# Kernel tuning notes

Measured on AMD Instinct MI355X. Metric: run time of the kernel, lower is better.

The kernel has to match this reference:

```python
import jax, jax.numpy as jnp
import numpy as np

EPS = 1e-5

def channel_norm(x):
    # per-(batch,channel) norm over spatial dims; torch.var default is unbiased (ddof=1)
    mn = x.mean(axis=(-1, -2), keepdims=True)
    std = jnp.sqrt(x.var(axis=(-1, -2), keepdims=True, ddof=1) + EPS)
    return (x - mn) / std

def conv1x1(x, W, b):
    # x: [B,C,H,W], W: [O,C], b: [O]
    return jnp.einsum('oc,bchw->bohw', W, x) + b[None, :, None, None]

def setup_inputs() -> dict:
    key = jax.random.key(0)
    ks = jax.random.split(key, 10)
    B, C, H, W = 4, 512, 64, 64
    s = 1.0 / np.sqrt(C)  # kaiming-uniform-ish scale for 1x1 conv
    inp = {
        'f_c': jax.random.normal(ks[0], (B, C, H, W), jnp.float32),
        'f_s': jax.random.normal(ks[1], (B, C, H, W), jnp.float32),
        'W_c1': jax.random.uniform(ks[2], (C, C), jnp.float32, -s, s),
        'b_c1': jax.random.uniform(ks[3], (C,), jnp.float32, -s, s),
        'W_s1': jax.random.uniform(ks[4], (C, C), jnp.float32, -s, s),
        'b_s1': jax.random.uniform(ks[5], (C,), jnp.float32, -s, s),
        'W_s2': jax.random.uniform(ks[6], (C, C), jnp.float32, -s, s),
        'b_s2': jax.random.uniform(ks[7], (C,), jnp.float32, -s, s),
        'W_csc': jax.random.uniform(ks[8], (C, C), jnp.float32, -s, s),
        'b_csc': jax.random.uniform(ks[9], (C,), jnp.float32, -s, s),
    }
    return inp

def reference(f_c, f_s, W_c1, b_c1, W_s1, b_s1, W_s2, b_s2, W_csc, b_csc):
    B, C, H, W = f_c.shape
    f_c_hat = channel_norm(f_c)
    f_s_hat = channel_norm(f_s)
    f = conv1x1(f_c_hat, W_c1, b_c1).reshape(B, C, H * W)  # queries [B,C,N]
    g = conv1x1(f_s_hat, W_s1, b_s1).reshape(B, C, H * W)  # keys    [B,C,N]
    scores = jnp.einsum('bci,bcj->bij', f, g)              # [B,N,N]
    attention = jax.nn.softmax(scores, axis=-1)
    h = conv1x1(f_s_hat, W_s2, b_s2).reshape(B, C, H * W)  # values  [B,C,N]
    out = jnp.einsum('bcj,bij->bci', h, attention).reshape(B, C, H, W)
    return conv1x1(out, W_csc, b_csc) + f_c
```

## Files before the change

### kernel.cpp

```cpp
#include <hip/hip_runtime.h>

typedef unsigned short u16;
typedef __attribute__((ext_vector_type(8))) _Float16 f16x8;
typedef __attribute__((ext_vector_type(16))) float f32x16;

#define N_SP 4096
#define C_CH 512
#define B_SZ 4

struct PtrTab { u16* p[4]; };

__device__ __forceinline__ u16 f2h(float f) {
    union { _Float16 h; u16 u; } x; x.h = (_Float16)f; return x.u;
}
__device__ __forceinline__ float h2f(u16 u) {
    union { u16 u; _Float16 h; } x; x.u = u; return (float)x.h;
}
__device__ __forceinline__ void async_cp16(const void* g, void* l) {
    __builtin_amdgcn_global_load_lds((const __attribute__((address_space(1))) unsigned*)g,
                                     (__attribute__((address_space(3))) unsigned*)l, 16, 0, 0);
}
__device__ __forceinline__ float wave_reduce_sum(float v) {
    #pragma unroll
    for (int off = 32; off; off >>= 1) v += __shfl_xor(v, off, 64);
    return v;
}
__device__ __forceinline__ float wave_reduce_max(float v) {
    #pragma unroll
    for (int off = 32; off; off >>= 1) v = fmaxf(v, __shfl_xor(v, off, 64));
    return v;
}

__global__ __launch_bounds__(256) void transpose_cast_stats(
        const float* __restrict__ fc, const float* __restrict__ fs,
        u16* __restrict__ xc, u16* __restrict__ xs,
        float* __restrict__ part_s, float* __restrict__ part_ss) {
    __shared__ float tile[64][65];
    const int t = threadIdx.x;
    const int n0 = blockIdx.x * 64, c0 = blockIdx.y * 64;
    const int z = blockIdx.z;
    const int b = z & 3, which = z >> 2;
    const float* src = which ? fs : fc;
    u16* dst = which ? xs : xc;
    const int r = t >> 4, q4 = (t & 15) * 4;
    #pragma unroll
    for (int it = 0; it < 4; ++it) {
        const int row = it * 16 + r;
        float4 v = *(const float4*)(src + ((size_t)b * C_CH + c0 + row) * N_SP + n0 + q4);
        tile[row][q4 + 0] = v.x; tile[row][q4 + 1] = v.y;
        tile[row][q4 + 2] = v.z; tile[row][q4 + 3] = v.w;
    }
    __syncthreads();
    {
        const int cr = t >> 2, q = t & 3;
        float s = 0.f, ss = 0.f;
        #pragma unroll
        for (int i = 0; i < 16; ++i) {
            float a = tile[cr][q * 16 + i];
            s += a; ss += a * a;
        }
        s += __shfl_xor(s, 1, 64);  s += __shfl_xor(s, 2, 64);
        ss += __shfl_xor(ss, 1, 64); ss += __shfl_xor(ss, 2, 64);
        if (q == 0) {
            atomicAdd(&part_s[z * 512 + c0 + cr], s);
            atomicAdd(&part_ss[z * 512 + c0 + cr], ss);
        }
    }
    #pragma unroll
    for (int it = 0; it < 4; ++it) {
        const int nrow = it * 16 + r;
        ushort4 h4;
        h4.x = f2h(tile[q4 + 0][nrow]);
        h4.y = f2h(tile[q4 + 1][nrow]);
        h4.z = f2h(tile[q4 + 2][nrow]);
        h4.w = f2h(tile[q4 + 3][nrow]);
        *(ushort4*)(dst + ((size_t)b * N_SP + n0 + nrow) * C_CH + c0 + q4) = h4;
    }
}

__global__ __launch_bounds__(256) void prep1(
        const float* __restrict__ W_c1, const float* __restrict__ W_s1,
        const float* __restrict__ W_s2, const float* __restrict__ W_csc,
        const float* __restrict__ b_c1, const float* __restrict__ b_s2,
        const float* __restrict__ b_csc,
        u16* __restrict__ Wbase,
        const float* __restrict__ part_s, const float* __restrict__ part_ss,
        float* __restrict__ mu_a, float* __restrict__ rs_a,
        float* __restrict__ w_u, float* __restrict__ bfold0) {
    __shared__ float tile[64][65];
    const int t = threadIdx.x, z = blockIdx.z;
    if (z < 4) {
        const int n0 = blockIdx.x * 64, c0 = blockIdx.y * 64;
        const float* W = (z == 0) ? W_c1 : (z == 1) ? W_s1 : (z == 2) ? W_s2 : W_csc;
        u16* D = Wbase + ((z == 0) ? 2 : (z == 1) ? 0 : (z == 2) ? 3 : 1) * 262144;
        const int r = t >> 4, q4 = (t & 15) * 4;
        #pragma unroll
        for (int it = 0; it < 4; ++it) {
            const int row = it * 16 + r;
            float4 v = *(const float4*)(W + (size_t)(c0 + row) * 512 + n0 + q4);
            if (z == 3) {
                ushort4 h4 = { f2h(v.x), f2h(v.y), f2h(v.z), f2h(v.w) };
                *(ushort4*)(D + (size_t)(c0 + row) * 512 + n0 + q4) = h4;
            } else {
                tile[row][q4 + 0] = v.x; tile[row][q4 + 1] = v.y;
                tile[row][q4 + 2] = v.z; tile[row][q4 + 3] = v.w;
            }
        }
        __syncthreads();
        if (z == 3) return;
        #pragma unroll
        for (int it = 0; it < 4; ++it) {
            const int nrow = it * 16 + r;
            ushort4 h4;
            h4.x = f2h(tile[q4 + 0][nrow]);
            h4.y = f2h(tile[q4 + 1][nrow]);
            h4.z = f2h(tile[q4 + 2][nrow]);
            h4.w = f2h(tile[q4 + 3][nrow]);
            *(ushort4*)(D + (size_t)(n0 + nrow) * 512 + c0 + q4) = h4;
        }
        return;
    }
    const int flat = blockIdx.y * 8 + blockIdx.x;
    if (flat < 8) {
        #pragma unroll
        for (int h = 0; h < 2; ++h) {
            const int c = flat * 512 + h * 256 + t;
            const float S = part_s[c], SS = part_ss[c];
            const float mean = S * (1.f / N_SP);
            const float var = (SS - S * mean) * (1.f / (N_SP - 1));
            mu_a[c] = mean;
            rs_a[c] = rsqrtf(var + 1e-5f);
        }
    } else if (flat < 10) {
        const int d = (flat - 8) * 256 + t;
        float acc = 0.f;
        for (int o = 0; o < 512; ++o) acc += b_c1[o] * W_s1[(size_t)o * 512 + d];
        w_u[d] = acc;
    } else if (flat < 42) {
        const int w4 = t >> 6, l = t & 63;
        #pragma unroll
        for (int q = 0; q < 4; ++q) {
            const int o = (flat - 10) * 16 + w4 * 4 + q;
            const float4 w0 = *(const float4*)(W_csc + (size_t)o * 512 + l * 8);
            const float4 w1 = *(const float4*)(W_csc + (size_t)o * 512 + l * 8 + 4);
            const float4 b0 = *(const float4*)(b_s2 + l * 8);
            const float4 b1 = *(const float4*)(b_s2 + l * 8 + 4);
            float acc = w0.x * b0.x + w0.y * b0.y + w0.z * b0.z + w0.w * b0.w
                      + w1.x * b1.x + w1.y * b1.y + w1.z * b1.z + w1.w * b1.w;
            acc = wave_reduce_sum(acc);
            if (l == 0) bfold0[o] = acc + b_csc[o];
        }
    }
}

__global__ __launch_bounds__(256) void prep2(
        const u16* __restrict__ WqT16, const u16* __restrict__ Wf16,
        const u16* __restrict__ xs,
        const float* __restrict__ mu_a, const float* __restrict__ rs_a,
        const float* __restrict__ bfold0, const float* __restrict__ w_u,
        u16* __restrict__ Wq_z, u16* __restrict__ Wf_z,
        float* __restrict__ bq, float* __restrict__ bh, float* __restrict__ u_) {
    const int id = blockIdx.x, t = threadIdx.x;
    if (id < 1024) {
        const int y = id >> 9;
        const size_t e = ((size_t)(id & 511) * 256 + t) * 8;
        const int z = (int)(e >> 18), rem = (int)(e & 262143);
        const int d = rem >> 9, a0 = rem & 511;
        u16 v[8];
        if (y == 0) {
            *(uint4*)v = *(const uint4*)(WqT16 + rem);
            const float rd = rs_a[(4 + z) * 512 + d];
            const float* rc = rs_a + z * 512 + a0;
            #pragma unroll
            for (int i = 0; i < 8; ++i) v[i] = f2h(h2f(v[i]) * rc[i] * rd);
            *(uint4*)(Wq_z + e) = *(const uint4*)v;
        } else {
            *(uint4*)v = *(const uint4*)(Wf16 + rem);
            const float* rk = rs_a + (4 + z) * 512 + a0;
            #pragma unroll
            for (int i = 0; i < 8; ++i) v[i] = f2h(h2f(v[i]) * rk[i]);
            *(uint4*)(Wf_z + e) = *(const uint4*)v;
        }
    } else if (id < 2048) {
        const int w = t >> 6, l = t & 63;
        const int oid = (id - 1024) * 4 + w;
        const int kind = oid >> 11;
        const int z = (oid >> 9) & 3, d = oid & 511;
        const u16* row = (kind == 0 ? WqT16 : Wf16) + (size_t)d * 512;
        const int sb = (kind == 0 ? z : 4 + z) * 512;
        float acc = 0.f;
        #pragma unroll
        for (int i = 0; i < 8; ++i) {
            const int a = l * 8 + i;
            acc += h2f(row[a]) * mu_a[sb + a] * rs_a[sb + a];
        }
        acc = wave_reduce_sum(acc);
        if (l == 0) {
            if (kind == 0) bq[z * 512 + d] = -acc * rs_a[(4 + z) * 512 + d];
            else           bh[z * 512 + d] = bfold0[d] - acc;
        }
    } else {
        const int id2 = id - 2048;
        const int b = id2 >> 6, xblk = id2 & 63;
        const int w = t >> 6, l = t & 63;
        float4 u0 = *(const float4*)(w_u + l * 8);
        float4 u1 = *(const float4*)(w_u + l * 8 + 4);
        const float4 r0 = *(const float4*)(rs_a + (4 + b) * 512 + l * 8);
        const float4 r1 = *(const float4*)(rs_a + (4 + b) * 512 + l * 8 + 4);
        u0.x *= r0.x; u0.y *= r0.y; u0.z *= r0.z; u0.w *= r0.w;
        u1.x *= r1.x; u1.y *= r1.y; u1.z *= r1.z; u1.w *= r1.w;
        #pragma unroll
        for (int jj = 0; jj < 16; ++jj) {
            const int j = xblk * 64 + w * 16 + jj;
            const u16* row = xs + ((size_t)b * N_SP + j) * C_CH + l * 8;
            f16x8 x = *(const f16x8*)row;
            float acc = (float)x[0] * u0.x + (float)x[1] * u0.y + (float)x[2] * u0.z + (float)x[3] * u0.w
                      + (float)x[4] * u1.x + (float)x[5] * u1.y + (float)x[6] * u1.z + (float)x[7] * u1.w;
            acc = wave_reduce_sum(acc);
            if (l == 0) u_[(size_t)b * N_SP + j] = acc;
        }
    }
}

enum { OUT_F32 = 0, OUT_F16 = 1 };

template<int OUTMODE, bool TABB, bool TABD, int MI, int MJ>
__global__ __launch_bounds__(256) void gemm_bt(
    const u16* __restrict__ A, const u16* __restrict__ B, PtrTab tab,
    float* __restrict__ Df, u16* __restrict__ Dh,
    const float* __restrict__ bias_m, const float* __restrict__ bias_n,
    const float* __restrict__ res,
    int M, int N, int K, int lda, int ldb, int ldd,
    size_t sA, size_t sB, size_t sD, size_t sR, int sBm, int sBn)
{
    constexpr int TM = MI * 64, TN = MJ * 64, BK = 64;
    constexpr int AITS = (TM * BK) / (256 * 8);
    constexpr int BITS = (TN * BK) / (256 * 8);
    __shared__ u16 smem[(TM + TN) * BK];
    u16* As = smem;
    u16* Bs = smem + TM * BK;

    const int t = threadIdx.x;
    const int l = t & 63, w = t >> 6;
    const int m0 = blockIdx.y * TM, n0 = blockIdx.x * TN;
    const size_t zb = blockIdx.z;
    const u16* pA = A + zb * sA + (size_t)m0 * lda;
    const u16* pB = (TABB ? tab.p[zb] : B + zb * sB) + (size_t)n0 * ldb;

    const int wr = (w & 1) * (MI * 32), wc = (w >> 1) * (MJ * 32);

    f32x16 acc[MI][MJ] = {};

    for (int k0 = 0; k0 < K; k0 += BK) {
        #pragma unroll
        for (int it = 0; it < AITS; ++it) {
            const int L = it * 256 + t;
            const int row = L >> 3, c = L & 7;
            const int sc = (c ^ (row & 7)) * 8;
            async_cp16(pA + (size_t)row * lda + k0 + sc, As + L * 8);
        }
        #pragma unroll
        for (int it = 0; it < BITS; ++it) {
            const int L = it * 256 + t;
            const int row = L >> 3, c = L & 7;
            const int sc = (c ^ (row & 7)) * 8;
            async_cp16(pB + (size_t)row * ldb + k0 + sc, Bs + L * 8);
        }
        __syncthreads();
        #pragma unroll
        for (int kk = 0; kk < 4; ++kk) {
            f16x8 af[MI], bf[MJ];
            #pragma unroll
            for (int i = 0; i < MI; ++i) {
                const int row = wr + i * 32 + (l & 31);
                const int ch = ((kk * 2 + (l >> 5)) ^ (row & 7)) * 8;
                af[i] = *(const f16x8*)(As + row * BK + ch);
            }
            #pragma unroll
            for (int j = 0; j < MJ; ++j) {
                const int row = wc + j * 32 + (l & 31);
                const int ch = ((kk * 2 + (l >> 5)) ^ (row & 7)) * 8;
                bf[j] = *(const f16x8*)(Bs + row * BK + ch);
            }
            #pragma unroll
            for (int i = 0; i < MI; ++i)
                #pragma unroll
                for (int j = 0; j < MJ; ++j)
                    acc[i][j] = __builtin_amdgcn_mfma_f32_32x32x16_f16(af[i], bf[j], acc[i][j], 0, 0, 0);
        }
        __syncthreads();
    }

    const int cl = l & 31, rh = (l >> 5) * 4;
    u16* pDh = (OUTMODE == OUT_F16) ? (TABD ? tab.p[zb] : Dh + zb * sD) : nullptr;
    float* pDf = (OUTMODE == OUT_F32) ? (Df + zb * sD) : nullptr;
    #pragma unroll
    for (int i = 0; i < MI; ++i) {
        #pragma unroll
        for (int j = 0; j < MJ; ++j) {
            const int nn = n0 + wc + j * 32 + cl;
            const float bn = bias_n ? bias_n[(size_t)sBn * zb + nn] : 0.f;
            #pragma unroll
            for (int reg = 0; reg < 16; ++reg) {
                const int ml = (reg & 3) + 8 * (reg >> 2) + rh;
                const int mm = m0 + wr + i * 32 + ml;
                float v = acc[i][j][reg] + bn;
                if (bias_m) v += bias_m[(size_t)sBm * zb + mm];
                const size_t off = (size_t)mm * ldd + nn;
                if (OUTMODE == OUT_F32) {
                    if (res) v += res[zb * sR + off];
                    pDf[off] = v;
                } else {
                    pDh[off] = f2h(v);
                }
            }
        }
    }
}

__global__ __launch_bounds__(256) void softmax_kernel(PtrTab tab) {
    u16* row = tab.p[blockIdx.y] + (size_t)blockIdx.x * N_SP;
    const int t = threadIdx.x;
    u16 raw[16];
    *(uint4*)(raw + 0) = *(const uint4*)(row + t * 16);
    *(uint4*)(raw + 8) = *(const uint4*)(row + t * 16 + 8);
    float v[16];
    float mx = -1e30f;
    #pragma unroll
    for (int i = 0; i < 16; ++i) { v[i] = h2f(raw[i]); mx = fmaxf(mx, v[i]); }
    mx = wave_reduce_max(mx);
    __shared__ float red[4];
    const int wave = t >> 6;
    if ((t & 63) == 0) red[wave] = mx;
    __syncthreads();
    mx = fmaxf(fmaxf(red[0], red[1]), fmaxf(red[2], red[3]));
    float sum = 0.f;
    #pragma unroll
    for (int i = 0; i < 16; ++i) { v[i] = __expf(v[i] - mx); sum += v[i]; }
    sum = wave_reduce_sum(sum);
    __syncthreads();
    if ((t & 63) == 0) red[wave] = sum;
    __syncthreads();
    const float inv = 1.f / (red[0] + red[1] + red[2] + red[3]);
    #pragma unroll
    for (int i = 0; i < 16; ++i) raw[i] = f2h(v[i] * inv);
    *(uint4*)(row + t * 16)     = *(const uint4*)(raw + 0);
    *(uint4*)(row + t * 16 + 8) = *(const uint4*)(raw + 8);
}

extern "C" void kernel_launch(void* const* d_in, const int* in_sizes, int n_in,
                              void* d_out, int out_size, void* d_ws, size_t ws_size,
                              hipStream_t stream) {
    const float* f_c   = (const float*)d_in[0];
    const float* f_s   = (const float*)d_in[1];
    const float* W_c1  = (const float*)d_in[2];
    const float* b_c1  = (const float*)d_in[3];
    const float* W_s1  = (const float*)d_in[4];
    const float* b_s1  = (const float*)d_in[5]; (void)b_s1;
    const float* W_s2  = (const float*)d_in[6];
    const float* b_s2  = (const float*)d_in[7];
    const float* W_csc = (const float*)d_in[8];
    const float* b_csc = (const float*)d_in[9];

    const size_t PB = (size_t)N_SP * C_CH;
    const size_t M1 = 1024 * 1024;

    u16* ws   = (u16*)d_ws;
    u16* Xs   = ws;
    u16* q_   = ws + 8 * M1;
    u16* hc   = ws + 16 * M1;
    u16* Xc   = ws + 24 * M1;
    u16* S3   = ws + 24 * M1;
    u16* S0   = ws + 40 * M1;
    u16* S1   = ws + 56 * M1;
    u16* S2   = ws + 72 * M1;
    u16* Wbase= ws + 88 * M1;
    u16* WqT16= Wbase + 4 * 262144;
    u16* Wf16 = Wbase + 5 * 262144;
    u16* Wq_z = Wbase + 6 * 262144;
    u16* Wf_z = Wq_z + 1048576;
    float* f32b = (float*)(ws + 92 * M1);
    float* part_s  = f32b;
    float* part_ss = f32b + 4096;
    float* mu_a    = f32b + 8192;
    float* rs_a    = f32b + 12288;
    float* w_u     = f32b + 16384;
    float* bfold0  = f32b + 16896;
    float* bq      = f32b + 17408;
    float* bh      = f32b + 19456;
    float* u_      = f32b + 21504;

    PtrTab Stab; Stab.p[0] = S0; Stab.p[1] = S1; Stab.p[2] = S2; Stab.p[3] = S3;
    PtrTab tab0 = Stab;

    hipMemsetAsync(part_s, 0, 2 * 4096 * sizeof(float), stream);

    transpose_cast_stats<<<dim3(64, 8, 8), 256, 0, stream>>>(f_c, f_s, Xc, Xs, part_s, part_ss);

    prep1<<<dim3(8, 8, 5), 256, 0, stream>>>(W_c1, W_s1, W_s2, W_csc, b_c1, b_s2, b_csc,
                                             Wbase, part_s, part_ss, mu_a, rs_a, w_u, bfold0);

    gemm_bt<OUT_F16, false, false, 2, 2><<<dim3(4, 4, 2), 256, 0, stream>>>(
        Wbase, Wbase + 2 * 262144, tab0, nullptr, WqT16, nullptr, nullptr, nullptr,
        512, 512, 512, 512, 512, 512, 262144, 262144, 262144, 0, 0, 0);

    prep2<<<2304, 256, 0, stream>>>(WqT16, Wf16, Xs, mu_a, rs_a, bfold0, w_u,
                                    Wq_z, Wf_z, bq, bh, u_);

    gemm_bt<OUT_F16, false, false, 1, 2><<<dim3(4, 64, B_SZ), 256, 0, stream>>>(
        Xc, Wq_z, tab0, nullptr, q_, nullptr, bq, nullptr,
        N_SP, C_CH, C_CH, C_CH, C_CH, C_CH, PB, 262144, PB, 0, 0, 512);
    gemm_bt<OUT_F16, false, false, 1, 2><<<dim3(32, 8, B_SZ), 256, 0, stream>>>(
        Wf_z, Xs, tab0, nullptr, hc, bh, nullptr, nullptr,
        C_CH, N_SP, C_CH, C_CH, C_CH, N_SP, 262144, PB, PB, 0, 512, 0);

    gemm_bt<OUT_F16, false, true, 2, 2><<<dim3(32, 32, B_SZ), 256, 0, stream>>>(
        q_, Xs, Stab, nullptr, nullptr, nullptr, u_, nullptr,
        N_SP, N_SP, C_CH, C_CH, C_CH, N_SP, PB, PB, 0, 0, 0, N_SP);

    softmax_kernel<<<dim3(N_SP, B_SZ), 256, 0, stream>>>(Stab);

    gemm_bt<OUT_F32, true, false, 1, 2><<<dim3(32, 8, B_SZ), 256, 0, stream>>>(
        hc, nullptr, Stab, (float*)d_out, nullptr, nullptr, nullptr, f_c,
        C_CH, N_SP, N_SP, N_SP, N_SP, N_SP, PB, 0, PB, PB, 0, 0);
}
```

Baseline: 440.2 us.

## Add double-buffered 512-thread GEMM with large tiles for scores and output

Adds a new GEMM kernel that uses 512 threads, 256x256 or 128x256 tiles, and a double-buffered LDS pipeline fed by async global-to-LDS copies with manual vmcnt waits and barriers. It replaces the previous GEMM for the two big attention GEMMs: scores (q·Xs^T) and output (hc·softmax^T plus residual). The larger tiles raise data reuse per load, and overlapping the next tile's load with the current MFMA work is meant to hide memory latency. In exchange it uses more registers and LDS per block, which may limit occupancy, and the output GEMM launches only 256 blocks.

```diff
diff --git a/kernel.cpp b/kernel.cpp
--- a/kernel.cpp
+++ b/kernel.cpp
@@ -29,6 +29,14 @@
     #pragma unroll
     for (int off = 32; off; off >>= 1) v = fmaxf(v, __shfl_xor(v, off, 64));
     return v;
+}
+__device__ __forceinline__ void bar() { asm volatile("s_barrier" ::: "memory"); }
+template<int N> __device__ __forceinline__ void vmwait() {
+    if constexpr (N == 0)  asm volatile("s_waitcnt vmcnt(0)" ::: "memory");
+    else if constexpr (N == 4)  asm volatile("s_waitcnt vmcnt(4)" ::: "memory");
+    else if constexpr (N == 6)  asm volatile("s_waitcnt vmcnt(6)" ::: "memory");
+    else if constexpr (N == 8)  asm volatile("s_waitcnt vmcnt(8)" ::: "memory");
+    else if constexpr (N == 12) asm volatile("s_waitcnt vmcnt(12)" ::: "memory");
 }
 
 __global__ __launch_bounds__(256) void transpose_cast_stats(
@@ -306,6 +314,118 @@
                 const int mm = m0 + wr + i * 32 + ml;
                 float v = acc[i][j][reg] + bn;
                 if (bias_m) v += bias_m[(size_t)sBm * zb + mm];
+                const size_t off = (size_t)mm * ldd + nn;
+                if (OUTMODE == OUT_F32) {
+                    if (res) v += res[zb * sR + off];
+                    pDf[off] = v;
+                } else {
+                    pDh[off] = f2h(v);
+                }
+            }
+        }
+    }
+}
+
+template<int OUTMODE, bool TABB, bool TABD, int BM, int BN>
+__global__ __launch_bounds__(512, 2) void gemm_db(
+    const u16* __restrict__ A, const u16* __restrict__ B, PtrTab tab,
+    float* __restrict__ Df, u16* __restrict__ Dh,
+    const float* __restrict__ bias_n, const float* __restrict__ res,
+    int K, int lda, int ldb, int ldd,
+    size_t sA, size_t sB, size_t sD, size_t sR, int sBn)
+{
+    constexpr int BK = 64;
+    constexpr int AITS = (BM * BK) / (512 * 8);
+    constexpr int BITS = (BN * BK) / (512 * 8);
+    constexpr int LTOT = AITS + BITS;
+    constexpr int LDSH = (BM + BN) * BK;
+    constexpr int MI_W = BM / 64;
+    constexpr int NJ_W = BN / 128;
+    __shared__ u16 smem[2 * LDSH];
+
+    const int t = threadIdx.x;
+    const int l = t & 63, w = t >> 6;
+    const int m0 = blockIdx.y * BM, n0 = blockIdx.x * BN;
+    const size_t zb = blockIdx.z;
+    const u16* pA = A + zb * sA + (size_t)m0 * lda;
+    const u16* pB = (TABB ? tab.p[zb] : B + zb * sB) + (size_t)n0 * ldb;
+
+    const int wmo = (w & 1) * (BM / 2);
+    const int wno = (w >> 1) * (BN / 4);
+
+    f32x16 acc[MI_W][NJ_W] = {};
+
+    auto stage = [&](int buf, int k0) {
+        u16* As_ = smem + buf * LDSH;
+        u16* Bs_ = As_ + BM * BK;
+        #pragma unroll
+        for (int it = 0; it < AITS; ++it) {
+            const int L = it * 512 + t;
+            const int row = L >> 3, c = L & 7;
+            const int sc = (c ^ (row & 7)) * 8;
+            async_cp16(pA + (size_t)row * lda + k0 + sc, As_ + L * 8);
+        }
+        #pragma unroll
+        for (int it = 0; it < BITS; ++it) {
+            const int L = it * 512 + t;
+            const int row = L >> 3, c = L & 7;
+            const int sc = (c ^ (row & 7)) * 8;
+            async_cp16(pB + (size_t)row * ldb + k0 + sc, Bs_ + L * 8);
+        }
+    };
+
+    const int NT = K / BK;
+    stage(0, 0);
+    for (int tl = 0; tl < NT; ++tl) {
+        bar();
+        if (tl + 1 < NT) {
+            stage((tl + 1) & 1, (tl + 1) * BK);
+            vmwait<LTOT>();
+        } else {
+            vmwait<0>();
+        }
+        bar();
+        const u16* As = smem + (tl & 1) * LDSH;
+        const u16* Bs = As + BM * BK;
+        #pragma unroll
+        for (int kk = 0; kk < 4; ++kk) {
+            f16x8 af[MI_W], bf[NJ_W];
+            #pragma unroll
+            for (int i = 0; i < MI_W; ++i) {
+                const int row = wmo + i * 32 + (l & 31);
+                const int ch = ((kk * 2 + (l >> 5)) ^ (row & 7)) * 8;
+                af[i] = *(const f16x8*)(As + row * BK + ch);
+            }
+            #pragma unroll
+            for (int j = 0; j < NJ_W; ++j) {
+                const int row = wno + j * 32 + (l & 31);
+                const int ch = ((kk * 2 + (l >> 5)) ^ (row & 7)) * 8;
+                bf[j] = *(const f16x8*)(Bs + row * BK + ch);
+            }
+            __builtin_amdgcn_s_setprio(1);
+            #pragma unroll
+            for (int i = 0; i < MI_W; ++i)
+                #pragma unroll
+                for (int j = 0; j < NJ_W; ++j)
+                    acc[i][j] = __builtin_amdgcn_mfma_f32_32x32x16_f16(af[i], bf[j], acc[i][j], 0, 0, 0);
+            __builtin_amdgcn_s_setprio(0);
+        }
+    }
+
+    const int cl = l & 31, rh = (l >> 5) * 4;
+    u16* pDh = (OUTMODE == OUT_F16) ? (TABD ? tab.p[zb] : Dh + zb * sD) : nullptr;
+    float* pDf = (OUTMODE == OUT_F32) ? (Df + zb * sD) : nullptr;
+    #pragma unroll
+    for (int i = 0; i < MI_W; ++i) {
+        #pragma unroll
+        for (int j = 0; j < NJ_W; ++j) {
+            const int nn = n0 + wno + j * 32 + cl;
+            const float bn = bias_n ? bias_n[(size_t)sBn * zb + nn] : 0.f;
+            #pragma unroll
+            for (int reg = 0; reg < 16; ++reg) {
+                const int ml = (reg & 3) + 8 * (reg >> 2) + rh;
+                const int mm = m0 + wmo + i * 32 + ml;
+                float v = acc[i][j][reg] + bn;
                 const size_t off = (size_t)mm * ldd + nn;
                 if (OUTMODE == OUT_F32) {
                     if (res) v += res[zb * sR + off];
@@ -414,13 +534,13 @@
         Wf_z, Xs, tab0, nullptr, hc, bh, nullptr, nullptr,
         C_CH, N_SP, C_CH, C_CH, C_CH, N_SP, 262144, PB, PB, 0, 512, 0);
 
-    gemm_bt<OUT_F16, false, true, 2, 2><<<dim3(32, 32, B_SZ), 256, 0, stream>>>(
-        q_, Xs, Stab, nullptr, nullptr, nullptr, u_, nullptr,
-        N_SP, N_SP, C_CH, C_CH, C_CH, N_SP, PB, PB, 0, 0, 0, N_SP);
+    gemm_db<OUT_F16, false, true, 256, 256><<<dim3(16, 16, B_SZ), 512, 0, stream>>>(
+        q_, Xs, Stab, nullptr, nullptr, u_, nullptr,
+        C_CH, C_CH, C_CH, N_SP, PB, PB, 0, 0, N_SP);
 
     softmax_kernel<<<dim3(N_SP, B_SZ), 256, 0, stream>>>(Stab);
 
-    gemm_bt<OUT_F32, true, false, 1, 2><<<dim3(32, 8, B_SZ), 256, 0, stream>>>(
-        hc, nullptr, Stab, (float*)d_out, nullptr, nullptr, nullptr, f_c,
-        C_CH, N_SP, N_SP, N_SP, N_SP, N_SP, PB, 0, PB, PB, 0, 0);
-}
+    gemm_db<OUT_F32, true, false, 128, 256><<<dim3(16, 4, B_SZ), 512, 0, stream>>>(
+        hc, nullptr, Stab, (float*)d_out, nullptr, nullptr, f_c,
+        N_SP, N_SP, N_SP, N_SP, PB, 0, PB, PB, 0);
+}
```

After: 443.3 us. Within noise of the previous version (+0.7%).

## Add gemm_s kernel using 16x16x32 MFMA with XOR-swizzled LDS tiles

Applied to the files above, without the earlier changes.

Adds a new GEMM kernel that uses 16x16x32 f16 MFMA fragments and stores LDS tiles with an XOR-swizzled chunk layout, filled by async global-to-LDS copies. All four large GEMMs (q projection, h projection, scores, output) now launch it instead of gemm_bt, with the same grid sizes. The aim is to cut LDS bank conflicts and use a faster MFMA shape. The kernel is single-buffered with two syncs per K step, so load latency may not be hidden as well as before.

```diff
diff --git a/kernel.cpp b/kernel.cpp
--- a/kernel.cpp
+++ b/kernel.cpp
@@ -2,6 +2,7 @@
 
 typedef unsigned short u16;
 typedef __attribute__((ext_vector_type(8))) _Float16 f16x8;
+typedef __attribute__((ext_vector_type(4))) float f32x4;
 typedef __attribute__((ext_vector_type(16))) float f32x16;
 
 #define N_SP 4096
@@ -305,6 +306,102 @@
                 const int ml = (reg & 3) + 8 * (reg >> 2) + rh;
                 const int mm = m0 + wr + i * 32 + ml;
                 float v = acc[i][j][reg] + bn;
+                if (bias_m) v += bias_m[(size_t)sBm * zb + mm];
+                const size_t off = (size_t)mm * ldd + nn;
+                if (OUTMODE == OUT_F32) {
+                    if (res) v += res[zb * sR + off];
+                    pDf[off] = v;
+                } else {
+                    pDh[off] = f2h(v);
+                }
+            }
+        }
+    }
+}
+
+template<int OUTMODE, bool TABB, bool TABD, int MI>
+__global__ __launch_bounds__(256) void gemm_s(
+    const u16* __restrict__ A, const u16* __restrict__ B, PtrTab tab,
+    float* __restrict__ Df, u16* __restrict__ Dh,
+    const float* __restrict__ bias_m, const float* __restrict__ bias_n,
+    const float* __restrict__ res,
+    int K, int lda, int ldb, int ldd,
+    size_t sA, size_t sB, size_t sD, size_t sR, int sBm, int sBn)
+{
+    constexpr int TM = MI * 64, TN = 128, BK = 64;
+    constexpr int AF = 2 * MI;
+    constexpr int AITS = (TM * BK) / (256 * 8);
+    constexpr int BITS = (TN * BK) / (256 * 8);
+    __shared__ u16 smem[(TM + TN) * BK];
+    u16* As = smem;
+    u16* Bs = smem + TM * BK;
+
+    const int t = threadIdx.x;
+    const int l = t & 63, w = t >> 6;
+    const int m0 = blockIdx.y * TM, n0 = blockIdx.x * TN;
+    const size_t zb = blockIdx.z;
+    const u16* pA = A + zb * sA + (size_t)m0 * lda;
+    const u16* pB = (TABB ? tab.p[zb] : B + zb * sB) + (size_t)n0 * ldb;
+
+    const int wr = (w & 1) * (AF * 16);
+    const int wc = (w >> 1) * 64;
+
+    f32x4 acc[AF][4] = {};
+
+    for (int k0 = 0; k0 < K; k0 += BK) {
+        #pragma unroll
+        for (int it = 0; it < AITS; ++it) {
+            const int L = it * 256 + t;
+            const int row = L >> 3, c = L & 7;
+            const int sc = (c ^ (row & 7)) * 8;
+            async_cp16(pA + (size_t)row * lda + k0 + sc, As + row * BK + c * 8);
+        }
+        #pragma unroll
+        for (int it = 0; it < BITS; ++it) {
+            const int L = it * 256 + t;
+            const int row = L >> 3, c = L & 7;
+            const int sc = (c ^ (row & 7)) * 8;
+            async_cp16(pB + (size_t)row * ldb + k0 + sc, Bs + row * BK + c * 8);
+        }
+        __syncthreads();
+        #pragma unroll
+        for (int kk = 0; kk < 2; ++kk) {
+            f16x8 af[AF], bf[4];
+            #pragma unroll
+            for (int mf = 0; mf < AF; ++mf) {
+                const int row = wr + mf * 16 + (l & 15);
+                const int ch = (kk * 4 + (l >> 4)) ^ (row & 7);
+                af[mf] = *(const f16x8*)(As + row * BK + ch * 8);
+            }
+            #pragma unroll
+            for (int nf = 0; nf < 4; ++nf) {
+                const int row = wc + nf * 16 + (l & 15);
+                const int ch = (kk * 4 + (l >> 4)) ^ (row & 7);
+                bf[nf] = *(const f16x8*)(Bs + row * BK + ch * 8);
+            }
+            #pragma unroll
+            for (int mf = 0; mf < AF; ++mf)
+                #pragma unroll
+                for (int nf = 0; nf < 4; ++nf)
+                    acc[mf][nf] = __builtin_amdgcn_mfma_f32_16x16x32_f16(af[mf], bf[nf], acc[mf][nf], 0, 0, 0);
+        }
+        __syncthreads();
+    }
+
+    const int cl = l & 15, rh = (l >> 4) * 4;
+    u16* pDh = (OUTMODE == OUT_F16) ? (TABD ? tab.p[zb] : Dh + zb * sD) : nullptr;
+    float* pDf = (OUTMODE == OUT_F32) ? (Df + zb * sD) : nullptr;
+    #pragma unroll
+    for (int mf = 0; mf < AF; ++mf) {
+        #pragma unroll
+        for (int nf = 0; nf < 4; ++nf) {
+            const int nn = n0 + wc + nf * 16 + cl;
+            const float bn = bias_n ? bias_n[(size_t)sBn * zb + nn] : 0.f;
+            const f32x4 a4 = acc[mf][nf];
+            #pragma unroll
+            for (int reg = 0; reg < 4; ++reg) {
+                const int mm = m0 + wr + mf * 16 + rh + reg;
+                float v = a4[reg] + bn;
                 if (bias_m) v += bias_m[(size_t)sBm * zb + mm];
                 const size_t off = (size_t)mm * ldd + nn;
                 if (OUTMODE == OUT_F32) {
@@ -407,20 +504,20 @@
     prep2<<<2304, 256, 0, stream>>>(WqT16, Wf16, Xs, mu_a, rs_a, bfold0, w_u,
                                     Wq_z, Wf_z, bq, bh, u_);
 
-    gemm_bt<OUT_F16, false, false, 1, 2><<<dim3(4, 64, B_SZ), 256, 0, stream>>>(
+    gemm_s<OUT_F16, false, false, 1><<<dim3(4, 64, B_SZ), 256, 0, stream>>>(
         Xc, Wq_z, tab0, nullptr, q_, nullptr, bq, nullptr,
-        N_SP, C_CH, C_CH, C_CH, C_CH, C_CH, PB, 262144, PB, 0, 0, 512);
-    gemm_bt<OUT_F16, false, false, 1, 2><<<dim3(32, 8, B_SZ), 256, 0, stream>>>(
+        C_CH, C_CH, C_CH, C_CH, PB, 262144, PB, 0, 0, 512);
+    gemm_s<OUT_F16, false, false, 1><<<dim3(32, 8, B_SZ), 256, 0, stream>>>(
         Wf_z, Xs, tab0, nullptr, hc, bh, nullptr, nullptr,
-        C_CH, N_SP, C_CH, C_CH, C_CH, N_SP, 262144, PB, PB, 0, 512, 0);
-
-    gemm_bt<OUT_F16, false, true, 2, 2><<<dim3(32, 32, B_SZ), 256, 0, stream>>>(
+        C_CH, C_CH, C_CH, N_SP, 262144, PB, PB, 0, 512, 0);
+
+    gemm_s<OUT_F16, false, true, 2><<<dim3(32, 32, B_SZ), 256, 0, stream>>>(
         q_, Xs, Stab, nullptr, nullptr, nullptr, u_, nullptr,
-        N_SP, N_SP, C_CH, C_CH, C_CH, N_SP, PB, PB, 0, 0, 0, N_SP);
+        C_CH, C_CH, C_CH, N_SP, PB, PB, 0, 0, 0, N_SP);
 
     softmax_kernel<<<dim3(N_SP, B_SZ), 256, 0, stream>>>(Stab);
 
-    gemm_bt<OUT_F32, true, false, 1, 2><<<dim3(32, 8, B_SZ), 256, 0, stream>>>(
+    gemm_s<OUT_F32, true, false, 1><<<dim3(32, 8, B_SZ), 256, 0, stream>>>(
         hc, nullptr, Stab, (float*)d_out, nullptr, nullptr, nullptr, f_c,
-        C_CH, N_SP, N_SP, N_SP, N_SP, N_SP, PB, 0, PB, PB, 0, 0);
-}
+        N_SP, N_SP, N_SP, N_SP, PB, 0, PB, PB, 0, 0);
+}
```

Measured after the change: 426.6 us. -3.1%, faster.
